# Performance work log

Measured on AMD Instinct MI355X. Metric: run time of the kernel, lower is better.

The kernel has to match this reference:

```python
import jax, jax.numpy as jnp
import numpy as np

N_HOPS = 3
EDGE_RATE = 0.5   # quirk: floor(rate+u)==1 KEEPS an edge with prob=rate, scaled by 1/(1-rate)
MESS_RATE = 0.1   # standard dropout: zero with prob p, scale kept by 1/(1-p)
N_USERS = 50000
N_ITEMS = 100000
N_NODES = N_USERS + N_ITEMS
NNZ = 1000000
D = 64


def setup_inputs() -> dict:
    key = jax.random.key(0)
    k_u, k_i, k_r, k_c, k_v = jax.random.split(key, 5)
    return {
        "user_embed": jax.random.normal(k_u, (N_USERS, D), dtype=jnp.float32),
        "item_embed": jax.random.normal(k_i, (N_ITEMS, D), dtype=jnp.float32),
        "rows": jax.random.randint(k_r, (NNZ,), 0, N_NODES),
        "cols": jax.random.randint(k_c, (NNZ,), 0, N_NODES),
        "vals": jax.random.uniform(k_v, (NNZ,), dtype=jnp.float32),
    }


def reference(user_embed, item_embed, rows, cols, vals):
    n_users = user_embed.shape[0]
    n_nodes = n_users + item_embed.shape[0]

    all_embed = jnp.concatenate([user_embed, item_embed], axis=0)  # [N, D]
    agg = all_embed
    embs = [all_embed]

    key = jax.random.key(42)
    for hop in range(N_HOPS):
        key, k_e, k_m = jax.random.split(key, 3)
        # edge dropout (faithful to torch._sparse_dropout): keep iff floor(rate+u)==1
        u = jax.random.uniform(k_e, (vals.shape[0],), dtype=vals.dtype)
        keep = (EDGE_RATE + u) >= 1.0
        v = jnp.where(keep, vals, jnp.zeros_like(vals)) * (1.0 / (1.0 - EDGE_RATE))
        # SpMM: out[r] += v * agg[c]  (zeroed edges contribute nothing, same math as
        # rebuilding a smaller sparse tensor, without dynamic shapes)
        msgs = v[:, None] * agg[cols]                       # [nnz, D]
        agg = jax.ops.segment_sum(msgs, rows, num_segments=n_nodes)
        # message dropout (nn.Dropout): zero with prob p, scale kept by 1/(1-p)
        m = jax.random.bernoulli(k_m, 1.0 - MESS_RATE, agg.shape)
        agg = jnp.where(m, agg / (1.0 - MESS_RATE), jnp.zeros_like(agg))
        embs.append(agg)

    embs = jnp.stack(embs, axis=1)  # [N, n_hops+1, D]
    return embs[:n_users], embs[n_users:]
```

## Files before the change

### kernel.cpp

```cpp
#include <hip/hip_runtime.h>
#include <stdint.h>


static constexpr int kUsers = 50000;
static constexpr int kItems = 100000;
static constexpr int kNodes = kUsers + kItems;
static constexpr int kNnz   = 1000000;
static constexpr int kD     = 64;
static constexpr int kHops  = 3;
static constexpr int kRowF  = (kHops + 1) * kD;

static constexpr int kScanBlocks = 147;
static constexpr int kCntN       = kScanBlocks * 1024;

__host__ __device__ inline void tf2x32(uint32_t k0, uint32_t k1,
                                       uint32_t x0, uint32_t x1,
                                       uint32_t &o0, uint32_t &o1) {
  uint32_t ks2 = k0 ^ k1 ^ 0x1BD11BDAu;
  x0 += k0; x1 += k1;
#define TF_R(r) { x0 += x1; x1 = (x1 << (r)) | (x1 >> (32 - (r))); x1 ^= x0; }
  TF_R(13) TF_R(15) TF_R(26) TF_R(6)   x0 += k1;  x1 += ks2 + 1u;
  TF_R(17) TF_R(29) TF_R(16) TF_R(24)  x0 += ks2; x1 += k0 + 2u;
  TF_R(13) TF_R(15) TF_R(26) TF_R(6)   x0 += k0;  x1 += k1 + 3u;
  TF_R(17) TF_R(29) TF_R(16) TF_R(24)  x0 += k1;  x1 += ks2 + 4u;
  TF_R(13) TF_R(15) TF_R(26) TF_R(6)   x0 += ks2; x1 += k0 + 5u;
#undef TF_R
  o0 = x0; o1 = x1;
}

__device__ inline uint32_t jax_bits32(uint32_t k0, uint32_t k1, uint32_t i) {
  uint32_t b1, b2;
  tf2x32(k0, k1, 0u, i, b1, b2);
  return b1 ^ b2;
}

__device__ inline float bits_to_unit(uint32_t b) {
  return __uint_as_float((b >> 9) | 0x3f800000u) - 1.0f;
}


__global__ __launch_bounds__(256) void init_slice0(
    const float4* __restrict__ user, const float4* __restrict__ item,
    float4* __restrict__ out, int4* __restrict__ cnt4) {
  int i = blockIdx.x * 256 + threadIdx.x;
  if (i < kCntN / 4) cnt4[i] = make_int4(0, 0, 0, 0);
  if (i >= kNodes * 16) return;
  int node = i >> 4, q = i & 15;
  float4 v = (node < kUsers) ? user[node * 16 + q]
                             : item[(node - kUsers) * 16 + q];
  out[(size_t)node * (kRowF / 4) + q] = v;
}

__global__ __launch_bounds__(256) void hist_kernel(
    const int* __restrict__ rows, int* __restrict__ cnt) {
  int e = blockIdx.x * 256 + threadIdx.x;
  if (e >= kNnz) return;
  atomicAdd(&cnt[rows[e]], 1);
}

__global__ __launch_bounds__(256) void scanA(
    const int* __restrict__ cnt, int* __restrict__ partials) {
  int t = threadIdx.x;
  int4 v = ((const int4*)(cnt + blockIdx.x * 1024))[t];
  int s = v.x + v.y + v.z + v.w;
  __shared__ int sh[256];
  sh[t] = s; __syncthreads();
  for (int off = 128; off > 0; off >>= 1) {
    if (t < off) sh[t] += sh[t + off];
    __syncthreads();
  }
  if (t == 0) partials[blockIdx.x] = sh[0];
}

__global__ __launch_bounds__(256) void scanB(int* __restrict__ partials) {
  int t = threadIdx.x;
  int v = (t < kScanBlocks) ? partials[t] : 0;
  __shared__ int sh[256];
  sh[t] = v; __syncthreads();
  for (int off = 1; off < 256; off <<= 1) {
    int a = (t >= off) ? sh[t - off] : 0;
    __syncthreads();
    sh[t] += a;
    __syncthreads();
  }
  if (t < kScanBlocks) partials[t] = sh[t] - v;
}

__global__ __launch_bounds__(256) void scanC(
    const int* __restrict__ cnt, const int* __restrict__ partials,
    int* __restrict__ X) {
  int t = threadIdx.x;
  int4 v = ((const int4*)(cnt + blockIdx.x * 1024))[t];
  int s = v.x + v.y + v.z + v.w;
  __shared__ int sh[256];
  sh[t] = s; __syncthreads();
  for (int off = 1; off < 256; off <<= 1) {
    int a = (t >= off) ? sh[t - off] : 0;
    __syncthreads();
    sh[t] += a;
    __syncthreads();
  }
  int base = partials[blockIdx.x] + sh[t] - s;
  int4 o;
  o.x = base; o.y = base + v.x; o.z = o.y + v.y; o.w = o.z + v.z;
  ((int4*)(X + blockIdx.x * 1024))[t] = o;
}

__global__ __launch_bounds__(256) void scatter_kernel(
    const int* __restrict__ rows, const int* __restrict__ cols,
    const float* __restrict__ vals, int* __restrict__ X,
    uint2* __restrict__ ed,
    uint32_t e00, uint32_t e01, uint32_t e10, uint32_t e11,
    uint32_t e20, uint32_t e21) {
  int e = blockIdx.x * 256 + threadIdx.x;
  if (e >= kNnz) return;
  int r = rows[e];
  int pos = atomicAdd(&X[r], 1);
  float u0 = bits_to_unit(jax_bits32(e00, e01, (uint32_t)e));
  float u1 = bits_to_unit(jax_bits32(e10, e11, (uint32_t)e));
  float u2 = bits_to_unit(jax_bits32(e20, e21, (uint32_t)e));
  uint32_t packed = (uint32_t)cols[e]
                  | ((0.5f + u0 >= 1.0f) ? (1u << 29) : 0u)
                  | ((0.5f + u1 >= 1.0f) ? (1u << 30) : 0u)
                  | ((0.5f + u2 >= 1.0f) ? (1u << 31) : 0u);
  ed[pos] = make_uint2(packed, __float_as_uint(vals[e] * 2.0f));
}

__global__ __launch_bounds__(256) void csr_spmm(
    const int* __restrict__ X, const uint2* __restrict__ ed,
    float* __restrict__ out, int hop, uint32_t km0, uint32_t km1) {
  int pair = blockIdx.x * 4 + (threadIdx.x >> 6);
  int rA = pair * 2;
  if (rA >= kNodes) return;
  int lane = threadIdx.x & 63;
  int g = lane >> 3, q = lane & 7;
  int sA = (rA == 0) ? 0 : X[rA - 1];
  int tA = X[rA];
  int tB = X[rA + 1];
  float4 a0 = make_float4(0.f, 0.f, 0.f, 0.f);
  float4 a1 = make_float4(0.f, 0.f, 0.f, 0.f);
  float4 b0 = make_float4(0.f, 0.f, 0.f, 0.f);
  float4 b1 = make_float4(0.f, 0.f, 0.f, 0.f);
  const float* src = out + (size_t)hop * kD;
  const uint32_t kbit = 1u << (29 + hop);
  int iA = sA + g, iB = tA + g;
  while (iA < tA || iB < tB) {
    if (iA < tA) {
      uint2 m = ed[iA];
      if (m.x & kbit) {
        float v = __uint_as_float(m.y);
        const float* p = src + (size_t)(m.x & 0x3FFFFu) * kRowF + (q << 3);
        float4 x0 = *(const float4*)p;
        float4 x1 = *(const float4*)(p + 4);
        a0.x += v * x0.x; a0.y += v * x0.y; a0.z += v * x0.z; a0.w += v * x0.w;
        a1.x += v * x1.x; a1.y += v * x1.y; a1.z += v * x1.z; a1.w += v * x1.w;
      }
      iA += 8;
    }
    if (iB < tB) {
      uint2 m = ed[iB];
      if (m.x & kbit) {
        float v = __uint_as_float(m.y);
        const float* p = src + (size_t)(m.x & 0x3FFFFu) * kRowF + (q << 3);
        float4 x0 = *(const float4*)p;
        float4 x1 = *(const float4*)(p + 4);
        b0.x += v * x0.x; b0.y += v * x0.y; b0.z += v * x0.z; b0.w += v * x0.w;
        b1.x += v * x1.x; b1.y += v * x1.y; b1.z += v * x1.z; b1.w += v * x1.w;
      }
      iB += 8;
    }
  }
#pragma unroll
  for (int msk = 8; msk <= 32; msk <<= 1) {
    a0.x += __shfl_xor(a0.x, msk); a0.y += __shfl_xor(a0.y, msk);
    a0.z += __shfl_xor(a0.z, msk); a0.w += __shfl_xor(a0.w, msk);
    a1.x += __shfl_xor(a1.x, msk); a1.y += __shfl_xor(a1.y, msk);
    a1.z += __shfl_xor(a1.z, msk); a1.w += __shfl_xor(a1.w, msk);
    b0.x += __shfl_xor(b0.x, msk); b0.y += __shfl_xor(b0.y, msk);
    b0.z += __shfl_xor(b0.z, msk); b0.w += __shfl_xor(b0.w, msk);
    b1.x += __shfl_xor(b1.x, msk); b1.y += __shfl_xor(b1.y, msk);
    b1.z += __shfl_xor(b1.z, msk); b1.w += __shfl_xor(b1.w, msk);
  }
  float uA = bits_to_unit(jax_bits32(km0, km1, (uint32_t)(rA * kD + lane)));
  float uB = bits_to_unit(jax_bits32(km0, km1, (uint32_t)((rA + 1) * kD + lane)));
  float mA = (uA < 0.9f) ? (1.0f / 0.9f) : 0.0f;
  float mB = (uB < 0.9f) ? (1.0f / 0.9f) : 0.0f;
  float w[8];
#pragma unroll
  for (int j = 0; j < 8; ++j) {
    float wA = __shfl(mA, (q << 3) + j);
    float wB = __shfl(mB, (q << 3) + j);
    w[j] = (g == 0) ? wA : wB;
  }
  if (g == 0) {
    float* dst = out + (size_t)rA * kRowF + (hop + 1) * kD + (q << 3);
    *(float4*)dst       = make_float4(a0.x * w[0], a0.y * w[1], a0.z * w[2], a0.w * w[3]);
    *(float4*)(dst + 4) = make_float4(a1.x * w[4], a1.y * w[5], a1.z * w[6], a1.w * w[7]);
  } else if (g == 1) {
    float* dst = out + (size_t)(rA + 1) * kRowF + (hop + 1) * kD + (q << 3);
    *(float4*)dst       = make_float4(b0.x * w[0], b0.y * w[1], b0.z * w[2], b0.w * w[3]);
    *(float4*)(dst + 4) = make_float4(b1.x * w[4], b1.y * w[5], b1.z * w[6], b1.w * w[7]);
  }
}

__global__ __launch_bounds__(256) void init_full(
    const float4* __restrict__ user, const float4* __restrict__ item,
    float4* __restrict__ out) {
  int i = blockIdx.x * 256 + threadIdx.x;
  if (i >= kNodes * 16) return;
  int node = i >> 4, q = i & 15;
  float4 v = (node < kUsers) ? user[node * 16 + q]
                             : item[(node - kUsers) * 16 + q];
  float4 z = make_float4(0.f, 0.f, 0.f, 0.f);
  float4* row = out + (size_t)node * (kRowF / 4);
  row[q] = v; row[16 + q] = z; row[32 + q] = z; row[48 + q] = z;
}

__global__ __launch_bounds__(256) void spmm_atomic(
    const int* __restrict__ rows, const int* __restrict__ cols,
    const float* __restrict__ vals, float* __restrict__ out, int hop,
    uint32_t k0, uint32_t k1) {
  int e = (int)((blockIdx.x * 256u + threadIdx.x) >> 6);
  if (e >= kNnz) return;
  int lane = threadIdx.x & 63;
  float u = bits_to_unit(jax_bits32(k0, k1, (uint32_t)e));
  if (!(0.5f + u >= 1.0f)) return;
  float v = vals[e] * 2.0f;
  int r = rows[e], c = cols[e];
  float msg = v * out[(size_t)c * kRowF + hop * kD + lane];
  atomicAdd(&out[(size_t)r * kRowF + (hop + 1) * kD + lane], msg);
}

__global__ __launch_bounds__(256) void mdrop_kernel(
    float* __restrict__ out, int hop, uint32_t k0, uint32_t k1) {
  const int total = kNodes * kD;
  int j = blockIdx.x * 256 + threadIdx.x;
  if (j >= total) return;
  float u = bits_to_unit(jax_bits32(k0, k1, (uint32_t)j));
  int node = j >> 6, d = j & 63;
  size_t idx = (size_t)node * kRowF + (hop + 1) * kD + d;
  float a = out[idx];
  out[idx] = (u < 0.9f) ? a / 0.9f : 0.0f;
}

extern "C" void kernel_launch(void* const* d_in, const int* in_sizes, int n_in,
                              void* d_out, int out_size, void* d_ws, size_t ws_size,
                              hipStream_t stream) {
  const float* user = (const float*)d_in[0];
  const float* item = (const float*)d_in[1];
  const int*   rows = (const int*)d_in[2];
  const int*   cols = (const int*)d_in[3];
  const float* vals = (const float*)d_in[4];
  float* out = (float*)d_out;

  uint32_t k0 = 0u, k1 = 42u;
  uint32_t ke[kHops][2], km[kHops][2];
  for (int hop = 0; hop < kHops; ++hop) {
    uint32_t n0, n1;
    tf2x32(k0, k1, 0u, 0u, n0, n1);
    tf2x32(k0, k1, 0u, 1u, ke[hop][0], ke[hop][1]);
    tf2x32(k0, k1, 0u, 2u, km[hop][0], km[hop][1]);
    k0 = n0; k1 = n1;
  }

  const size_t cnt_b = (size_t)kCntN * 4;
  const size_t x_b   = (size_t)kCntN * 4;
  const size_t ed_b  = (size_t)kNnz * 8;
  const size_t par_b = 1024;
  const size_t need  = cnt_b + x_b + ed_b + par_b;

  if (ws_size >= need) {
    char* ws = (char*)d_ws;
    int*   cnt      = (int*)ws;
    int*   X        = (int*)(ws + cnt_b);
    uint2* ed       = (uint2*)(ws + cnt_b + x_b);
    int*   partials = (int*)(ws + cnt_b + x_b + ed_b);

    init_slice0<<<(kNodes * 16 + 255) / 256, 256, 0, stream>>>(
        (const float4*)user, (const float4*)item, (float4*)out, (int4*)cnt);

    hist_kernel<<<(kNnz + 255) / 256, 256, 0, stream>>>(rows, cnt);
    scanA<<<kScanBlocks, 256, 0, stream>>>(cnt, partials);
    scanB<<<1, 256, 0, stream>>>(partials);
    scanC<<<kScanBlocks, 256, 0, stream>>>(cnt, partials, X);
    scatter_kernel<<<(kNnz + 255) / 256, 256, 0, stream>>>(
        rows, cols, vals, X, ed,
        ke[0][0], ke[0][1], ke[1][0], ke[1][1], ke[2][0], ke[2][1]);

    const int nPairs = kNodes / 2;
    for (int hop = 0; hop < kHops; ++hop) {
      csr_spmm<<<(nPairs + 3) / 4, 256, 0, stream>>>(
          X, ed, out, hop, km[hop][0], km[hop][1]);
    }
  } else {
    init_full<<<(kNodes * 16 + 255) / 256, 256, 0, stream>>>(
        (const float4*)user, (const float4*)item, (float4*)out);
    for (int hop = 0; hop < kHops; ++hop) {
      spmm_atomic<<<(kNnz * 64 + 255) / 256, 256, 0, stream>>>(
          rows, cols, vals, out, hop, ke[hop][0], ke[hop][1]);
      mdrop_kernel<<<(kNodes * kD + 255) / 256, 256, 0, stream>>>(
          out, hop, km[hop][0], km[hop][1]);
    }
  }
}
```

Measured before the change: 297.5 us.

## Build per-hop CSR of kept edges only and fuse histogram into init

Edge-dropout masks are now applied when the CSR is built. A separate row segment is created for each hop that holds only the kept edges, so the SpMM loop no longer walks dropped edges and no longer tests mask bits. The histogram is fused into the embedding-copy kernel and counts kept edges per hop. The scan runs over three concatenated count arrays, and a memset replaces the in-kernel zeroing. In exchange the scatter does up to three atomics and record writes per edge, and the edge buffer grows to a fixed capacity that assumes about half the edges survive each hop.

```diff
diff --git a/kernel.cpp b/kernel.cpp
--- a/kernel.cpp
+++ b/kernel.cpp
@@ -10,8 +10,10 @@
 static constexpr int kHops  = 3;
 static constexpr int kRowF  = (kHops + 1) * kD;
 
-static constexpr int kScanBlocks = 147;
-static constexpr int kCntN       = kScanBlocks * 1024;
+static constexpr int kCntN       = 147 * 1024;
+static constexpr int kScanBlocks = 3 * 147;
+static constexpr int kCntTotal   = kScanBlocks * 1024;
+static constexpr int kEdCap      = 1600000;
 
 __host__ __device__ inline void tf2x32(uint32_t k0, uint32_t k1,
                                        uint32_t x0, uint32_t x1,
@@ -39,23 +41,28 @@
 }
 
 
-__global__ __launch_bounds__(256) void init_slice0(
+__global__ __launch_bounds__(256) void init_hist(
     const float4* __restrict__ user, const float4* __restrict__ item,
-    float4* __restrict__ out, int4* __restrict__ cnt4) {
+    float4* __restrict__ out, const int* __restrict__ rows,
+    int* __restrict__ cnt,
+    uint32_t e00, uint32_t e01, uint32_t e10, uint32_t e11,
+    uint32_t e20, uint32_t e21) {
   int i = blockIdx.x * 256 + threadIdx.x;
-  if (i < kCntN / 4) cnt4[i] = make_int4(0, 0, 0, 0);
-  if (i >= kNodes * 16) return;
-  int node = i >> 4, q = i & 15;
-  float4 v = (node < kUsers) ? user[node * 16 + q]
-                             : item[(node - kUsers) * 16 + q];
-  out[(size_t)node * (kRowF / 4) + q] = v;
-}
-
-__global__ __launch_bounds__(256) void hist_kernel(
-    const int* __restrict__ rows, int* __restrict__ cnt) {
-  int e = blockIdx.x * 256 + threadIdx.x;
-  if (e >= kNnz) return;
-  atomicAdd(&cnt[rows[e]], 1);
+  if (i < kNodes * 16) {
+    int node = i >> 4, q = i & 15;
+    float4 v = (node < kUsers) ? user[node * 16 + q]
+                               : item[(node - kUsers) * 16 + q];
+    out[(size_t)node * (kRowF / 4) + q] = v;
+  }
+  if (i < kNnz) {
+    int r = rows[i];
+    float u0 = bits_to_unit(jax_bits32(e00, e01, (uint32_t)i));
+    float u1 = bits_to_unit(jax_bits32(e10, e11, (uint32_t)i));
+    float u2 = bits_to_unit(jax_bits32(e20, e21, (uint32_t)i));
+    if (0.5f + u0 >= 1.0f) atomicAdd(&cnt[r], 1);
+    if (0.5f + u1 >= 1.0f) atomicAdd(&cnt[kCntN + r], 1);
+    if (0.5f + u2 >= 1.0f) atomicAdd(&cnt[2 * kCntN + r], 1);
+  }
 }
 
 __global__ __launch_bounds__(256) void scanA(
@@ -72,12 +79,12 @@
   if (t == 0) partials[blockIdx.x] = sh[0];
 }
 
-__global__ __launch_bounds__(256) void scanB(int* __restrict__ partials) {
+__global__ __launch_bounds__(512) void scanB(int* __restrict__ partials) {
   int t = threadIdx.x;
   int v = (t < kScanBlocks) ? partials[t] : 0;
-  __shared__ int sh[256];
+  __shared__ int sh[512];
   sh[t] = v; __syncthreads();
-  for (int off = 1; off < 256; off <<= 1) {
+  for (int off = 1; off < 512; off <<= 1) {
     int a = (t >= off) ? sh[t - off] : 0;
     __syncthreads();
     sh[t] += a;
@@ -87,8 +94,7 @@
 }
 
 __global__ __launch_bounds__(256) void scanC(
-    const int* __restrict__ cnt, const int* __restrict__ partials,
-    int* __restrict__ X) {
+    int* __restrict__ cnt, const int* __restrict__ partials) {
   int t = threadIdx.x;
   int4 v = ((const int4*)(cnt + blockIdx.x * 1024))[t];
   int s = v.x + v.y + v.z + v.w;
@@ -103,7 +109,7 @@
   int base = partials[blockIdx.x] + sh[t] - s;
   int4 o;
   o.x = base; o.y = base + v.x; o.z = o.y + v.y; o.w = o.z + v.z;
-  ((int4*)(X + blockIdx.x * 1024))[t] = o;
+  ((int4*)(cnt + blockIdx.x * 1024))[t] = o;
 }
 
 __global__ __launch_bounds__(256) void scatter_kernel(
@@ -115,15 +121,22 @@
   int e = blockIdx.x * 256 + threadIdx.x;
   if (e >= kNnz) return;
   int r = rows[e];
-  int pos = atomicAdd(&X[r], 1);
+  uint2 rec = make_uint2((uint32_t)cols[e], __float_as_uint(vals[e] * 2.0f));
   float u0 = bits_to_unit(jax_bits32(e00, e01, (uint32_t)e));
   float u1 = bits_to_unit(jax_bits32(e10, e11, (uint32_t)e));
   float u2 = bits_to_unit(jax_bits32(e20, e21, (uint32_t)e));
-  uint32_t packed = (uint32_t)cols[e]
-                  | ((0.5f + u0 >= 1.0f) ? (1u << 29) : 0u)
-                  | ((0.5f + u1 >= 1.0f) ? (1u << 30) : 0u)
-                  | ((0.5f + u2 >= 1.0f) ? (1u << 31) : 0u);
-  ed[pos] = make_uint2(packed, __float_as_uint(vals[e] * 2.0f));
+  if (0.5f + u0 >= 1.0f) {
+    int pos = atomicAdd(&X[r], 1);
+    if (pos < kEdCap) ed[pos] = rec;
+  }
+  if (0.5f + u1 >= 1.0f) {
+    int pos = atomicAdd(&X[kCntN + r], 1);
+    if (pos < kEdCap) ed[pos] = rec;
+  }
+  if (0.5f + u2 >= 1.0f) {
+    int pos = atomicAdd(&X[2 * kCntN + r], 1);
+    if (pos < kEdCap) ed[pos] = rec;
+  }
 }
 
 __global__ __launch_bounds__(256) void csr_spmm(
@@ -134,39 +147,39 @@
   if (rA >= kNodes) return;
   int lane = threadIdx.x & 63;
   int g = lane >> 3, q = lane & 7;
-  int sA = (rA == 0) ? 0 : X[rA - 1];
-  int tA = X[rA];
-  int tB = X[rA + 1];
+  int idx0 = hop * kCntN + rA;
+  int sA = (idx0 == 0) ? 0 : X[idx0 - 1];
+  int tA = X[idx0];
+  int tB = X[idx0 + 1];
+  float uA = bits_to_unit(jax_bits32(km0, km1, (uint32_t)(rA * kD + lane)));
+  float uB = bits_to_unit(jax_bits32(km0, km1, (uint32_t)((rA + 1) * kD + lane)));
+  float mA = (uA < 0.9f) ? (1.0f / 0.9f) : 0.0f;
+  float mB = (uB < 0.9f) ? (1.0f / 0.9f) : 0.0f;
   float4 a0 = make_float4(0.f, 0.f, 0.f, 0.f);
   float4 a1 = make_float4(0.f, 0.f, 0.f, 0.f);
   float4 b0 = make_float4(0.f, 0.f, 0.f, 0.f);
   float4 b1 = make_float4(0.f, 0.f, 0.f, 0.f);
   const float* src = out + (size_t)hop * kD;
-  const uint32_t kbit = 1u << (29 + hop);
   int iA = sA + g, iB = tA + g;
   while (iA < tA || iB < tB) {
     if (iA < tA) {
       uint2 m = ed[iA];
-      if (m.x & kbit) {
-        float v = __uint_as_float(m.y);
-        const float* p = src + (size_t)(m.x & 0x3FFFFu) * kRowF + (q << 3);
-        float4 x0 = *(const float4*)p;
-        float4 x1 = *(const float4*)(p + 4);
-        a0.x += v * x0.x; a0.y += v * x0.y; a0.z += v * x0.z; a0.w += v * x0.w;
-        a1.x += v * x1.x; a1.y += v * x1.y; a1.z += v * x1.z; a1.w += v * x1.w;
-      }
+      float v = __uint_as_float(m.y);
+      const float* p = src + (size_t)m.x * kRowF + (q << 3);
+      float4 x0 = *(const float4*)p;
+      float4 x1 = *(const float4*)(p + 4);
+      a0.x += v * x0.x; a0.y += v * x0.y; a0.z += v * x0.z; a0.w += v * x0.w;
+      a1.x += v * x1.x; a1.y += v * x1.y; a1.z += v * x1.z; a1.w += v * x1.w;
       iA += 8;
     }
     if (iB < tB) {
       uint2 m = ed[iB];
-      if (m.x & kbit) {
-        float v = __uint_as_float(m.y);
-        const float* p = src + (size_t)(m.x & 0x3FFFFu) * kRowF + (q << 3);
-        float4 x0 = *(const float4*)p;
-        float4 x1 = *(const float4*)(p + 4);
-        b0.x += v * x0.x; b0.y += v * x0.y; b0.z += v * x0.z; b0.w += v * x0.w;
-        b1.x += v * x1.x; b1.y += v * x1.y; b1.z += v * x1.z; b1.w += v * x1.w;
-      }
+      float v = __uint_as_float(m.y);
+      const float* p = src + (size_t)m.x * kRowF + (q << 3);
+      float4 x0 = *(const float4*)p;
+      float4 x1 = *(const float4*)(p + 4);
+      b0.x += v * x0.x; b0.y += v * x0.y; b0.z += v * x0.z; b0.w += v * x0.w;
+      b1.x += v * x1.x; b1.y += v * x1.y; b1.z += v * x1.z; b1.w += v * x1.w;
       iB += 8;
     }
   }
@@ -181,10 +194,6 @@
     b1.x += __shfl_xor(b1.x, msk); b1.y += __shfl_xor(b1.y, msk);
     b1.z += __shfl_xor(b1.z, msk); b1.w += __shfl_xor(b1.w, msk);
   }
-  float uA = bits_to_unit(jax_bits32(km0, km1, (uint32_t)(rA * kD + lane)));
-  float uB = bits_to_unit(jax_bits32(km0, km1, (uint32_t)((rA + 1) * kD + lane)));
-  float mA = (uA < 0.9f) ? (1.0f / 0.9f) : 0.0f;
-  float mB = (uB < 0.9f) ? (1.0f / 0.9f) : 0.0f;
   float w[8];
 #pragma unroll
   for (int j = 0; j < 8; ++j) {
@@ -263,26 +272,24 @@
     k0 = n0; k1 = n1;
   }
 
-  const size_t cnt_b = (size_t)kCntN * 4;
-  const size_t x_b   = (size_t)kCntN * 4;
-  const size_t ed_b  = (size_t)kNnz * 8;
-  const size_t par_b = 1024;
-  const size_t need  = cnt_b + x_b + ed_b + par_b;
+  const size_t cnt_b = (size_t)kCntTotal * 4;
+  const size_t ed_b  = (size_t)kEdCap * 8;
+  const size_t par_b = 2048;
+  const size_t need  = cnt_b + ed_b + par_b;
 
   if (ws_size >= need) {
     char* ws = (char*)d_ws;
-    int*   cnt      = (int*)ws;
-    int*   X        = (int*)(ws + cnt_b);
-    uint2* ed       = (uint2*)(ws + cnt_b + x_b);
-    int*   partials = (int*)(ws + cnt_b + x_b + ed_b);
-
-    init_slice0<<<(kNodes * 16 + 255) / 256, 256, 0, stream>>>(
-        (const float4*)user, (const float4*)item, (float4*)out, (int4*)cnt);
-
-    hist_kernel<<<(kNnz + 255) / 256, 256, 0, stream>>>(rows, cnt);
-    scanA<<<kScanBlocks, 256, 0, stream>>>(cnt, partials);
-    scanB<<<1, 256, 0, stream>>>(partials);
-    scanC<<<kScanBlocks, 256, 0, stream>>>(cnt, partials, X);
+    int*   X        = (int*)ws;
+    uint2* ed       = (uint2*)(ws + cnt_b);
+    int*   partials = (int*)(ws + cnt_b + ed_b);
+
+    hipMemsetAsync(X, 0, cnt_b, stream);
+    init_hist<<<(kNodes * 16 + 255) / 256, 256, 0, stream>>>(
+        (const float4*)user, (const float4*)item, (float4*)out, rows, X,
+        ke[0][0], ke[0][1], ke[1][0], ke[1][1], ke[2][0], ke[2][1]);
+    scanA<<<kScanBlocks, 256, 0, stream>>>(X, partials);
+    scanB<<<1, 512, 0, stream>>>(partials);
+    scanC<<<kScanBlocks, 256, 0, stream>>>(X, partials);
     scatter_kernel<<<(kNnz + 255) / 256, 256, 0, stream>>>(
         rows, cols, vals, X, ed,
         ke[0][0], ke[0][1], ke[1][0], ke[1][1], ke[2][0], ke[2][1]);
```

After: 359.8 us. 20.9% more time.

## Gather from compact planar per-hop buffers and fuse init with histogram

Applied to the files above, without the earlier changes.

When the workspace is large enough, each hop now writes its output a second time into a dense [nodes, 64] ping-pong buffer. The next hop gathers neighbour rows from that buffer instead of from the interleaved 256-float output rows, which should make the random gathers far more cache-line dense. The slice-0 copy and the row histogram are merged into one kernel, and the scan now works in place on a single counter buffer that is cleared with a memset. The message-dropout random draw is also moved ahead of the edge loop. The cost is an extra 38 MB of writes per hop, about 77 MB of extra workspace, and behaviour that depends on the workspace size.

```diff
diff --git a/kernel.cpp b/kernel.cpp
--- a/kernel.cpp
+++ b/kernel.cpp
@@ -39,23 +39,19 @@
 }
 
 
-__global__ __launch_bounds__(256) void init_slice0(
+__global__ __launch_bounds__(256) void init_hist(
     const float4* __restrict__ user, const float4* __restrict__ item,
-    float4* __restrict__ out, int4* __restrict__ cnt4) {
+    float4* __restrict__ out, float4* __restrict__ planar0,
+    const int* __restrict__ rows, int* __restrict__ cnt) {
   int i = blockIdx.x * 256 + threadIdx.x;
-  if (i < kCntN / 4) cnt4[i] = make_int4(0, 0, 0, 0);
-  if (i >= kNodes * 16) return;
-  int node = i >> 4, q = i & 15;
-  float4 v = (node < kUsers) ? user[node * 16 + q]
-                             : item[(node - kUsers) * 16 + q];
-  out[(size_t)node * (kRowF / 4) + q] = v;
-}
-
-__global__ __launch_bounds__(256) void hist_kernel(
-    const int* __restrict__ rows, int* __restrict__ cnt) {
-  int e = blockIdx.x * 256 + threadIdx.x;
-  if (e >= kNnz) return;
-  atomicAdd(&cnt[rows[e]], 1);
+  if (i < kNodes * 16) {
+    int node = i >> 4, q = i & 15;
+    float4 v = (node < kUsers) ? user[node * 16 + q]
+                               : item[(node - kUsers) * 16 + q];
+    out[(size_t)node * (kRowF / 4) + q] = v;
+    if (planar0) planar0[i] = v;
+  }
+  if (i < kNnz) atomicAdd(&cnt[rows[i]], 1);
 }
 
 __global__ __launch_bounds__(256) void scanA(
@@ -87,8 +83,7 @@
 }
 
 __global__ __launch_bounds__(256) void scanC(
-    const int* __restrict__ cnt, const int* __restrict__ partials,
-    int* __restrict__ X) {
+    int* __restrict__ cnt, const int* __restrict__ partials) {
   int t = threadIdx.x;
   int4 v = ((const int4*)(cnt + blockIdx.x * 1024))[t];
   int s = v.x + v.y + v.z + v.w;
@@ -103,7 +98,7 @@
   int base = partials[blockIdx.x] + sh[t] - s;
   int4 o;
   o.x = base; o.y = base + v.x; o.z = o.y + v.y; o.w = o.z + v.z;
-  ((int4*)(X + blockIdx.x * 1024))[t] = o;
+  ((int4*)(cnt + blockIdx.x * 1024))[t] = o;
 }
 
 __global__ __launch_bounds__(256) void scatter_kernel(
@@ -128,7 +123,9 @@
 
 __global__ __launch_bounds__(256) void csr_spmm(
     const int* __restrict__ X, const uint2* __restrict__ ed,
-    float* __restrict__ out, int hop, uint32_t km0, uint32_t km1) {
+    const float* __restrict__ src, int srcStride,
+    float* __restrict__ dstI, float* __restrict__ dstP,
+    int hop, uint32_t km0, uint32_t km1) {
   int pair = blockIdx.x * 4 + (threadIdx.x >> 6);
   int rA = pair * 2;
   if (rA >= kNodes) return;
@@ -137,11 +134,14 @@
   int sA = (rA == 0) ? 0 : X[rA - 1];
   int tA = X[rA];
   int tB = X[rA + 1];
+  float uA = bits_to_unit(jax_bits32(km0, km1, (uint32_t)(rA * kD + lane)));
+  float uB = bits_to_unit(jax_bits32(km0, km1, (uint32_t)((rA + 1) * kD + lane)));
+  float mA = (uA < 0.9f) ? (1.0f / 0.9f) : 0.0f;
+  float mB = (uB < 0.9f) ? (1.0f / 0.9f) : 0.0f;
   float4 a0 = make_float4(0.f, 0.f, 0.f, 0.f);
   float4 a1 = make_float4(0.f, 0.f, 0.f, 0.f);
   float4 b0 = make_float4(0.f, 0.f, 0.f, 0.f);
   float4 b1 = make_float4(0.f, 0.f, 0.f, 0.f);
-  const float* src = out + (size_t)hop * kD;
   const uint32_t kbit = 1u << (29 + hop);
   int iA = sA + g, iB = tA + g;
   while (iA < tA || iB < tB) {
@@ -149,7 +149,7 @@
       uint2 m = ed[iA];
       if (m.x & kbit) {
         float v = __uint_as_float(m.y);
-        const float* p = src + (size_t)(m.x & 0x3FFFFu) * kRowF + (q << 3);
+        const float* p = src + (size_t)(m.x & 0x3FFFFu) * srcStride + (q << 3);
         float4 x0 = *(const float4*)p;
         float4 x1 = *(const float4*)(p + 4);
         a0.x += v * x0.x; a0.y += v * x0.y; a0.z += v * x0.z; a0.w += v * x0.w;
@@ -161,7 +161,7 @@
       uint2 m = ed[iB];
       if (m.x & kbit) {
         float v = __uint_as_float(m.y);
-        const float* p = src + (size_t)(m.x & 0x3FFFFu) * kRowF + (q << 3);
+        const float* p = src + (size_t)(m.x & 0x3FFFFu) * srcStride + (q << 3);
         float4 x0 = *(const float4*)p;
         float4 x1 = *(const float4*)(p + 4);
         b0.x += v * x0.x; b0.y += v * x0.y; b0.z += v * x0.z; b0.w += v * x0.w;
@@ -181,10 +181,6 @@
     b1.x += __shfl_xor(b1.x, msk); b1.y += __shfl_xor(b1.y, msk);
     b1.z += __shfl_xor(b1.z, msk); b1.w += __shfl_xor(b1.w, msk);
   }
-  float uA = bits_to_unit(jax_bits32(km0, km1, (uint32_t)(rA * kD + lane)));
-  float uB = bits_to_unit(jax_bits32(km0, km1, (uint32_t)((rA + 1) * kD + lane)));
-  float mA = (uA < 0.9f) ? (1.0f / 0.9f) : 0.0f;
-  float mB = (uB < 0.9f) ? (1.0f / 0.9f) : 0.0f;
   float w[8];
 #pragma unroll
   for (int j = 0; j < 8; ++j) {
@@ -192,14 +188,24 @@
     float wB = __shfl(mB, (q << 3) + j);
     w[j] = (g == 0) ? wA : wB;
   }
-  if (g == 0) {
-    float* dst = out + (size_t)rA * kRowF + (hop + 1) * kD + (q << 3);
-    *(float4*)dst       = make_float4(a0.x * w[0], a0.y * w[1], a0.z * w[2], a0.w * w[3]);
-    *(float4*)(dst + 4) = make_float4(a1.x * w[4], a1.y * w[5], a1.z * w[6], a1.w * w[7]);
-  } else if (g == 1) {
-    float* dst = out + (size_t)(rA + 1) * kRowF + (hop + 1) * kD + (q << 3);
-    *(float4*)dst       = make_float4(b0.x * w[0], b0.y * w[1], b0.z * w[2], b0.w * w[3]);
-    *(float4*)(dst + 4) = make_float4(b1.x * w[4], b1.y * w[5], b1.z * w[6], b1.w * w[7]);
+  if (g < 2) {
+    int r = rA + g;
+    float4 r0, r1;
+    if (g == 0) {
+      r0 = make_float4(a0.x * w[0], a0.y * w[1], a0.z * w[2], a0.w * w[3]);
+      r1 = make_float4(a1.x * w[4], a1.y * w[5], a1.z * w[6], a1.w * w[7]);
+    } else {
+      r0 = make_float4(b0.x * w[0], b0.y * w[1], b0.z * w[2], b0.w * w[3]);
+      r1 = make_float4(b1.x * w[4], b1.y * w[5], b1.z * w[6], b1.w * w[7]);
+    }
+    float* d1 = dstI + (size_t)r * kRowF + (q << 3);
+    *(float4*)d1 = r0;
+    *(float4*)(d1 + 4) = r1;
+    if (dstP) {
+      float* d2 = dstP + (size_t)r * kD + (q << 3);
+      *(float4*)d2 = r0;
+      *(float4*)(d2 + 4) = r1;
+    }
   }
 }
 
@@ -263,34 +269,50 @@
     k0 = n0; k1 = n1;
   }
 
-  const size_t cnt_b = (size_t)kCntN * 4;
-  const size_t x_b   = (size_t)kCntN * 4;
-  const size_t ed_b  = (size_t)kNnz * 8;
-  const size_t par_b = 1024;
-  const size_t need  = cnt_b + x_b + ed_b + par_b;
-
-  if (ws_size >= need) {
+  const size_t x_b    = (size_t)kCntN * 4;
+  const size_t ed_b   = ((size_t)kNnz * 8 + 4095) & ~(size_t)4095;
+  const size_t plan_b = (size_t)kNodes * kD * 4;
+  const size_t par_b  = 4096;
+  const size_t needB  = x_b + ed_b + par_b;
+  const size_t needA  = x_b + ed_b + 2 * plan_b + par_b;
+
+  if (ws_size >= needB) {
+    const bool planar = (ws_size >= needA);
     char* ws = (char*)d_ws;
-    int*   cnt      = (int*)ws;
-    int*   X        = (int*)(ws + cnt_b);
-    uint2* ed       = (uint2*)(ws + cnt_b + x_b);
-    int*   partials = (int*)(ws + cnt_b + x_b + ed_b);
-
-    init_slice0<<<(kNodes * 16 + 255) / 256, 256, 0, stream>>>(
-        (const float4*)user, (const float4*)item, (float4*)out, (int4*)cnt);
-
-    hist_kernel<<<(kNnz + 255) / 256, 256, 0, stream>>>(rows, cnt);
-    scanA<<<kScanBlocks, 256, 0, stream>>>(cnt, partials);
+    int*   X        = (int*)ws;
+    uint2* ed       = (uint2*)(ws + x_b);
+    float* planA    = planar ? (float*)(ws + x_b + ed_b) : nullptr;
+    float* planB    = planar ? (float*)(ws + x_b + ed_b + plan_b) : nullptr;
+    int*   partials = (int*)(ws + (planar ? needA : needB) - par_b);
+
+    hipMemsetAsync(X, 0, x_b, stream);
+    init_hist<<<(kNodes * 16 + 255) / 256, 256, 0, stream>>>(
+        (const float4*)user, (const float4*)item, (float4*)out,
+        (float4*)planA, rows, X);
+    scanA<<<kScanBlocks, 256, 0, stream>>>(X, partials);
     scanB<<<1, 256, 0, stream>>>(partials);
-    scanC<<<kScanBlocks, 256, 0, stream>>>(cnt, partials, X);
+    scanC<<<kScanBlocks, 256, 0, stream>>>(X, partials);
     scatter_kernel<<<(kNnz + 255) / 256, 256, 0, stream>>>(
         rows, cols, vals, X, ed,
         ke[0][0], ke[0][1], ke[1][0], ke[1][1], ke[2][0], ke[2][1]);
 
     const int nPairs = kNodes / 2;
     for (int hop = 0; hop < kHops; ++hop) {
-      csr_spmm<<<(nPairs + 3) / 4, 256, 0, stream>>>(
-          X, ed, out, hop, km[hop][0], km[hop][1]);
+      const float* src;
+      int srcStride;
+      float* dstP;
+      if (planar) {
+        src = (hop & 1) ? planB : planA;
+        srcStride = kD;
+        dstP = (hop == kHops - 1) ? nullptr : ((hop & 1) ? planA : planB);
+      } else {
+        src = out + (size_t)hop * kD;
+        srcStride = kRowF;
+        dstP = nullptr;
+      }
+      csr_spmm<<<nPairs / 4, 256, 0, stream>>>(
+          X, ed, src, srcStride, out + (size_t)(hop + 1) * kD, dstP,
+          hop, km[hop][0], km[hop][1]);
     }
   } else {
     init_full<<<(kNodes * 16 + 255) / 256, 256, 0, stream>>>(
```

Result: slower. 310.2 us (+4.3%).

## Split CSR scatter into record build plus row-range-partitioned routing pass

Applied to the files above, without the earlier changes.

Edge records (packed column, dropout bits, scaled value) are now built in edge order inside the histogram kernel. A new routing kernel scans chunks of rows eight times, once per row-range group, so each block scatters only into one eighth of the node range. The goal is better locality for the scatter atomics and writes. The scan now runs in place on the count array, removing the separate X buffer. The mask RNG in csr_spmm is also hoisted ahead of the gather loop, and the store branch is merged. In exchange, rows is read eight times and the rec buffer adds an extra 8 MB write and read.

```diff
diff --git a/kernel.cpp b/kernel.cpp
--- a/kernel.cpp
+++ b/kernel.cpp
@@ -12,6 +12,10 @@
 
 static constexpr int kScanBlocks = 147;
 static constexpr int kCntN       = kScanBlocks * 1024;
+
+static constexpr int kEPB     = 8192;
+static constexpr int kChunks  = (kNnz + kEPB - 1) / kEPB;
+static constexpr int kRowsPerGrp = kNodes / 8;
 
 __host__ __device__ inline void tf2x32(uint32_t k0, uint32_t k1,
                                        uint32_t x0, uint32_t x1,
@@ -51,11 +55,23 @@
   out[(size_t)node * (kRowF / 4) + q] = v;
 }
 
-__global__ __launch_bounds__(256) void hist_kernel(
-    const int* __restrict__ rows, int* __restrict__ cnt) {
+__global__ __launch_bounds__(256) void hist_rec(
+    const int* __restrict__ rows, const int* __restrict__ cols,
+    const float* __restrict__ vals, int* __restrict__ cnt,
+    uint2* __restrict__ rec,
+    uint32_t e00, uint32_t e01, uint32_t e10, uint32_t e11,
+    uint32_t e20, uint32_t e21) {
   int e = blockIdx.x * 256 + threadIdx.x;
   if (e >= kNnz) return;
   atomicAdd(&cnt[rows[e]], 1);
+  float u0 = bits_to_unit(jax_bits32(e00, e01, (uint32_t)e));
+  float u1 = bits_to_unit(jax_bits32(e10, e11, (uint32_t)e));
+  float u2 = bits_to_unit(jax_bits32(e20, e21, (uint32_t)e));
+  uint32_t packed = (uint32_t)cols[e]
+                  | ((0.5f + u0 >= 1.0f) ? (1u << 29) : 0u)
+                  | ((0.5f + u1 >= 1.0f) ? (1u << 30) : 0u)
+                  | ((0.5f + u2 >= 1.0f) ? (1u << 31) : 0u);
+  rec[e] = make_uint2(packed, __float_as_uint(vals[e] * 2.0f));
 }
 
 __global__ __launch_bounds__(256) void scanA(
@@ -87,8 +103,7 @@
 }
 
 __global__ __launch_bounds__(256) void scanC(
-    const int* __restrict__ cnt, const int* __restrict__ partials,
-    int* __restrict__ X) {
+    int* __restrict__ cnt, const int* __restrict__ partials) {
   int t = threadIdx.x;
   int4 v = ((const int4*)(cnt + blockIdx.x * 1024))[t];
   int s = v.x + v.y + v.z + v.w;
@@ -103,27 +118,34 @@
   int base = partials[blockIdx.x] + sh[t] - s;
   int4 o;
   o.x = base; o.y = base + v.x; o.z = o.y + v.y; o.w = o.z + v.z;
-  ((int4*)(X + blockIdx.x * 1024))[t] = o;
-}
-
-__global__ __launch_bounds__(256) void scatter_kernel(
-    const int* __restrict__ rows, const int* __restrict__ cols,
-    const float* __restrict__ vals, int* __restrict__ X,
-    uint2* __restrict__ ed,
-    uint32_t e00, uint32_t e01, uint32_t e10, uint32_t e11,
-    uint32_t e20, uint32_t e21) {
-  int e = blockIdx.x * 256 + threadIdx.x;
-  if (e >= kNnz) return;
-  int r = rows[e];
-  int pos = atomicAdd(&X[r], 1);
-  float u0 = bits_to_unit(jax_bits32(e00, e01, (uint32_t)e));
-  float u1 = bits_to_unit(jax_bits32(e10, e11, (uint32_t)e));
-  float u2 = bits_to_unit(jax_bits32(e20, e21, (uint32_t)e));
-  uint32_t packed = (uint32_t)cols[e]
-                  | ((0.5f + u0 >= 1.0f) ? (1u << 29) : 0u)
-                  | ((0.5f + u1 >= 1.0f) ? (1u << 30) : 0u)
-                  | ((0.5f + u2 >= 1.0f) ? (1u << 31) : 0u);
-  ed[pos] = make_uint2(packed, __float_as_uint(vals[e] * 2.0f));
+  ((int4*)(cnt + blockIdx.x * 1024))[t] = o;
+}
+
+__global__ __launch_bounds__(256) void route_scatter(
+    const int* __restrict__ rows, const uint2* __restrict__ rec,
+    int* __restrict__ X, uint2* __restrict__ ed) {
+  const int grp   = blockIdx.x & 7;
+  const int chunk = blockIdx.x >> 3;
+  const int lo = grp * kRowsPerGrp;
+  const int hi = lo + kRowsPerGrp;
+  const int base4 = chunk * (kEPB / 4);
+  const int t = threadIdx.x;
+#pragma unroll
+  for (int k = 0; k < kEPB / 4 / 256; ++k) {
+    int idx4 = base4 + k * 256 + t;
+    if (idx4 >= kNnz / 4) break;
+    int4 r4 = ((const int4*)rows)[idx4];
+    int e0 = idx4 * 4;
+    int rr[4] = {r4.x, r4.y, r4.z, r4.w};
+#pragma unroll
+    for (int j = 0; j < 4; ++j) {
+      int r = rr[j];
+      if (r >= lo && r < hi) {
+        int pos = atomicAdd(&X[r], 1);
+        ed[pos] = rec[e0 + j];
+      }
+    }
+  }
 }
 
 __global__ __launch_bounds__(256) void csr_spmm(
@@ -137,6 +159,10 @@
   int sA = (rA == 0) ? 0 : X[rA - 1];
   int tA = X[rA];
   int tB = X[rA + 1];
+  float uA = bits_to_unit(jax_bits32(km0, km1, (uint32_t)(rA * kD + lane)));
+  float uB = bits_to_unit(jax_bits32(km0, km1, (uint32_t)((rA + 1) * kD + lane)));
+  float mA = (uA < 0.9f) ? (1.0f / 0.9f) : 0.0f;
+  float mB = (uB < 0.9f) ? (1.0f / 0.9f) : 0.0f;
   float4 a0 = make_float4(0.f, 0.f, 0.f, 0.f);
   float4 a1 = make_float4(0.f, 0.f, 0.f, 0.f);
   float4 b0 = make_float4(0.f, 0.f, 0.f, 0.f);
@@ -181,10 +207,6 @@
     b1.x += __shfl_xor(b1.x, msk); b1.y += __shfl_xor(b1.y, msk);
     b1.z += __shfl_xor(b1.z, msk); b1.w += __shfl_xor(b1.w, msk);
   }
-  float uA = bits_to_unit(jax_bits32(km0, km1, (uint32_t)(rA * kD + lane)));
-  float uB = bits_to_unit(jax_bits32(km0, km1, (uint32_t)((rA + 1) * kD + lane)));
-  float mA = (uA < 0.9f) ? (1.0f / 0.9f) : 0.0f;
-  float mB = (uB < 0.9f) ? (1.0f / 0.9f) : 0.0f;
   float w[8];
 #pragma unroll
   for (int j = 0; j < 8; ++j) {
@@ -192,14 +214,19 @@
     float wB = __shfl(mB, (q << 3) + j);
     w[j] = (g == 0) ? wA : wB;
   }
-  if (g == 0) {
-    float* dst = out + (size_t)rA * kRowF + (hop + 1) * kD + (q << 3);
-    *(float4*)dst       = make_float4(a0.x * w[0], a0.y * w[1], a0.z * w[2], a0.w * w[3]);
-    *(float4*)(dst + 4) = make_float4(a1.x * w[4], a1.y * w[5], a1.z * w[6], a1.w * w[7]);
-  } else if (g == 1) {
-    float* dst = out + (size_t)(rA + 1) * kRowF + (hop + 1) * kD + (q << 3);
-    *(float4*)dst       = make_float4(b0.x * w[0], b0.y * w[1], b0.z * w[2], b0.w * w[3]);
-    *(float4*)(dst + 4) = make_float4(b1.x * w[4], b1.y * w[5], b1.z * w[6], b1.w * w[7]);
+  if (g < 2) {
+    int r = rA + g;
+    float4 r0, r1;
+    if (g == 0) {
+      r0 = make_float4(a0.x * w[0], a0.y * w[1], a0.z * w[2], a0.w * w[3]);
+      r1 = make_float4(a1.x * w[4], a1.y * w[5], a1.z * w[6], a1.w * w[7]);
+    } else {
+      r0 = make_float4(b0.x * w[0], b0.y * w[1], b0.z * w[2], b0.w * w[3]);
+      r1 = make_float4(b1.x * w[4], b1.y * w[5], b1.z * w[6], b1.w * w[7]);
+    }
+    float* dst = out + (size_t)r * kRowF + (hop + 1) * kD + (q << 3);
+    *(float4*)dst = r0;
+    *(float4*)(dst + 4) = r1;
   }
 }
 
@@ -263,29 +290,28 @@
     k0 = n0; k1 = n1;
   }
 
-  const size_t cnt_b = (size_t)kCntN * 4;
   const size_t x_b   = (size_t)kCntN * 4;
-  const size_t ed_b  = (size_t)kNnz * 8;
-  const size_t par_b = 1024;
-  const size_t need  = cnt_b + x_b + ed_b + par_b;
+  const size_t rec_b = ((size_t)kNnz * 8 + 4095) & ~(size_t)4095;
+  const size_t ed_b  = rec_b;
+  const size_t par_b = 4096;
+  const size_t need  = x_b + rec_b + ed_b + par_b;
 
   if (ws_size >= need) {
     char* ws = (char*)d_ws;
-    int*   cnt      = (int*)ws;
-    int*   X        = (int*)(ws + cnt_b);
-    uint2* ed       = (uint2*)(ws + cnt_b + x_b);
-    int*   partials = (int*)(ws + cnt_b + x_b + ed_b);
+    int*   X        = (int*)ws;
+    uint2* rec      = (uint2*)(ws + x_b);
+    uint2* ed       = (uint2*)(ws + x_b + rec_b);
+    int*   partials = (int*)(ws + x_b + rec_b + ed_b);
 
     init_slice0<<<(kNodes * 16 + 255) / 256, 256, 0, stream>>>(
-        (const float4*)user, (const float4*)item, (float4*)out, (int4*)cnt);
-
-    hist_kernel<<<(kNnz + 255) / 256, 256, 0, stream>>>(rows, cnt);
-    scanA<<<kScanBlocks, 256, 0, stream>>>(cnt, partials);
+        (const float4*)user, (const float4*)item, (float4*)out, (int4*)X);
+    hist_rec<<<(kNnz + 255) / 256, 256, 0, stream>>>(
+        rows, cols, vals, X, rec,
+        ke[0][0], ke[0][1], ke[1][0], ke[1][1], ke[2][0], ke[2][1]);
+    scanA<<<kScanBlocks, 256, 0, stream>>>(X, partials);
     scanB<<<1, 256, 0, stream>>>(partials);
-    scanC<<<kScanBlocks, 256, 0, stream>>>(cnt, partials, X);
-    scatter_kernel<<<(kNnz + 255) / 256, 256, 0, stream>>>(
-        rows, cols, vals, X, ed,
-        ke[0][0], ke[0][1], ke[1][0], ke[1][1], ke[2][0], ke[2][1]);
+    scanC<<<kScanBlocks, 256, 0, stream>>>(X, partials);
+    route_scatter<<<kChunks * 8, 256, 0, stream>>>(rows, rec, X, ed);
 
     const int nPairs = kNodes / 2;
     for (int hop = 0; hop < kHops; ++hop) {
```

Measured after the change: 270.7 us. -9.0%, faster.
